# Performance work log

Measured on AMD Instinct MI355X. Metric: run time of the kernel, lower is better.

## Reference

```python
import jax, jax.numpy as jnp
import numpy as np

TOP_K = 2  # hard-coded in MoCo.__init__ (self.top_k = 2)


def setup_inputs() -> dict:
    key = jax.random.key(0)
    k1, k2, k3 = jax.random.split(key, 3)
    B, D, E, O = 16384, 4096, 4, 256  # batch, mlp_dim, num_experts, dim
    v_standard = jax.random.normal(k1, (B, D), dtype=jnp.float32)
    router_w = jax.random.normal(k2, (D, E), dtype=jnp.float32) / np.float32(np.sqrt(D))
    expert_w = jax.random.normal(k3, (E, D, O), dtype=jnp.float32) / np.float32(np.sqrt(D))
    return {"v_standard": v_standard, "router_w": router_w, "expert_w": expert_w}


def reference(v_standard, router_w, expert_w):
    # Router + softmax gating: [B, E]
    routing_logits = v_standard @ router_w
    routing_weights = jax.nn.softmax(routing_logits, axis=-1)

    # Top-k gating, renormalized over the selected experts
    topk_weights, topk_indices = jax.lax.top_k(routing_weights, TOP_K)  # [B, k]
    topk_weights = topk_weights / topk_weights.sum(axis=-1, keepdims=True)

    # Dense all-expert compute (as in the original: every expert runs on every token)
    expert_outputs = jnp.einsum('bd,edo->beo', v_standard, expert_w)  # [B, E, O]

    # Gather the top-k expert outputs and combine with gate weights
    selected = jnp.take_along_axis(expert_outputs, topk_indices[:, :, None], axis=1)  # [B, k, O]
    moe_output = (selected * topk_weights[:, :, None]).sum(axis=1)  # [B, O]
    return moe_output, routing_weights
```

## Files before the change

### kernel.cpp

```cpp
#include <hip/hip_runtime.h>

typedef unsigned short ushort_t;
typedef __attribute__((ext_vector_type(8))) short short8;
typedef __attribute__((ext_vector_type(4))) float floatx4;
typedef __attribute__((ext_vector_type(4))) unsigned int uint4v;

static __device__ __forceinline__ unsigned short f2bf_rn(float f) {
  return (unsigned short)((__float_as_uint(f) + 0x8000u) >> 16);
}
static __device__ __forceinline__ unsigned int packbf(float a, float b) {
  return ((__float_as_uint(a) + 0x8000u) >> 16) |
         ((__float_as_uint(b) + 0x8000u) & 0xFFFF0000u);
}

__global__ __launch_bounds__(256) void k_transpose(const float* __restrict__ We,
                                                   ushort_t* __restrict__ WT) {
  __shared__ float tile[32][33];
  int t = threadIdx.x, tx = t & 31, ty = t >> 5;
  int d0 = blockIdx.x * 32, o0 = blockIdx.y * 32, e = blockIdx.z;
  const float* src = We + (size_t)e * 4096 * 256;
  ushort_t* dst = WT + (size_t)e * 256 * 4096;
#pragma unroll
  for (int r = 0; r < 4; ++r)
    tile[ty + r * 8][tx] = src[(size_t)(d0 + ty + r * 8) * 256 + (o0 + tx)];
  __syncthreads();
#pragma unroll
  for (int r = 0; r < 4; ++r)
    dst[(size_t)(o0 + ty + r * 8) * 4096 + (d0 + tx)] = f2bf_rn(tile[tx][ty + r * 8]);
}

__global__ __launch_bounds__(256) void k_prep_router(const float* __restrict__ Wr,
                                                     float* __restrict__ WrT32) {
  int d = blockIdx.x * 256 + threadIdx.x;
  float4 w = *(const float4*)(Wr + (size_t)d * 4);
  WrT32[d] = w.x;
  WrT32[4096 + d] = w.y;
  WrT32[2 * 4096 + d] = w.z;
  WrT32[3 * 4096 + d] = w.w;
}

__global__ __launch_bounds__(256) void k_routing(const float* __restrict__ V,
                                                 const float* __restrict__ WrT32,
                                                 float* __restrict__ rw_out,
                                                 float* __restrict__ gates) {
  int w = threadIdx.x >> 6, lane = threadIdx.x & 63;
  int b = blockIdx.x * 4 + w;
  const float* vrow = V + (size_t)b * 4096;
  float a0 = 0.f, a1 = 0.f, a2 = 0.f, a3 = 0.f;
#pragma unroll
  for (int j = 0; j < 16; ++j) {
    int d = j * 256 + lane * 4;
    float4 vv = *(const float4*)(vrow + d);
    float4 w0 = *(const float4*)(WrT32 + d);
    float4 w1 = *(const float4*)(WrT32 + 4096 + d);
    float4 w2 = *(const float4*)(WrT32 + 2 * 4096 + d);
    float4 w3 = *(const float4*)(WrT32 + 3 * 4096 + d);
    a0 += vv.x * w0.x + vv.y * w0.y + vv.z * w0.z + vv.w * w0.w;
    a1 += vv.x * w1.x + vv.y * w1.y + vv.z * w1.z + vv.w * w1.w;
    a2 += vv.x * w2.x + vv.y * w2.y + vv.z * w2.z + vv.w * w2.w;
    a3 += vv.x * w3.x + vv.y * w3.y + vv.z * w3.z + vv.w * w3.w;
  }
#pragma unroll
  for (int mask = 1; mask < 64; mask <<= 1) {
    a0 += __shfl_xor(a0, mask, 64);
    a1 += __shfl_xor(a1, mask, 64);
    a2 += __shfl_xor(a2, mask, 64);
    a3 += __shfl_xor(a3, mask, 64);
  }
  float mx = fmaxf(fmaxf(a0, a1), fmaxf(a2, a3));
  float e0 = expf(a0 - mx), e1 = expf(a1 - mx), e2 = expf(a2 - mx), e3 = expf(a3 - mx);
  float s = e0 + e1 + e2 + e3;
  float p[4] = {e0 / s, e1 / s, e2 / s, e3 / s};
  int i1 = 0;
#pragma unroll
  for (int k = 1; k < 4; ++k)
    if (p[k] > p[i1]) i1 = k;
  int i2 = (i1 == 0) ? 1 : 0;
#pragma unroll
  for (int k = 0; k < 4; ++k)
    if (k != i1 && p[k] > p[i2]) i2 = k;
  float gs = p[i1] + p[i2];
  if (lane < 4) {
    rw_out[(size_t)b * 4 + lane] = p[lane];
    gates[(size_t)b * 4 + lane] = (lane == i1 || lane == i2) ? (p[lane] / gs) : 0.f;
  }
}

#define BM 128
#define BN 64
#define BK 64

__global__ __launch_bounds__(256, 2) void k_gemm_moe(const float* __restrict__ V,
                                                     const ushort_t* __restrict__ WT,
                                                     const float* __restrict__ gates,
                                                     float* __restrict__ out) {
  const int Kd = 4096;
  int bn = blockIdx.x;
  int bm = blockIdx.y;
  int m0 = bm * BM, n0 = bn * BN;

  __shared__ __align__(16) ushort_t Asm[BM * BK];
  __shared__ __align__(16) ushort_t Bsm[4 * BN * BK];

  int t = threadIdx.x;
  int w = t >> 6, lane = t & 63;
  int quad = lane >> 4, mi = lane & 15;
  int wm = (w >> 1) * 64, wn = (w & 1) * 32;

  int aG[4], aL[4];
#pragma unroll
  for (int j = 0; j < 4; ++j) {
    int q = j * 256 + t;
    int row = q >> 3, c = q & 7;
    aG[j] = (m0 + row) * Kd + c * 8;
    aL[j] = (row * 8 + (c ^ (row & 7))) * 8;
  }
  int bG[8], bL[8];
#pragma unroll
  for (int j = 0; j < 8; ++j) {
    int q = j * 256 + t;
    int eb = q >> 9, rc = q & 511;
    int r = rc >> 3, c = rc & 7;
    bG[j] = eb * (256 * Kd) + (n0 + r) * Kd + c * 8;
    bL[j] = eb * (BN * BK) + (r * 8 + (c ^ (r & 7))) * 8;
  }

  int aOff[2][4], bOff[2][2];
#pragma unroll
  for (int k32 = 0; k32 < 2; ++k32) {
    int cc = k32 * 4 + quad;
#pragma unroll
    for (int i = 0; i < 4; ++i) {
      int rowa = wm + i * 16 + mi;
      aOff[k32][i] = (rowa * 8 + (cc ^ (rowa & 7))) * 8;
    }
#pragma unroll
    for (int j = 0; j < 2; ++j) {
      int rowb = wn + j * 16 + mi;
      bOff[k32][j] = (rowb * 8 + (cc ^ (rowb & 7))) * 8;
    }
  }

  floatx4 zero = {0.f, 0.f, 0.f, 0.f};
  floatx4 acc[4][4][2];
#pragma unroll
  for (int e = 0; e < 4; ++e)
#pragma unroll
    for (int i = 0; i < 4; ++i)
#pragma unroll
      for (int j = 0; j < 2; ++j) acc[e][i][j] = zero;

  float4 ax[4], ay[4];
  short8 bv[8];
#pragma unroll
  for (int j = 0; j < 4; ++j) {
    const float* ap = V + (size_t)aG[j];
    ax[j] = *(const float4*)ap;
    ay[j] = *(const float4*)(ap + 4);
  }
#pragma unroll
  for (int j = 0; j < 8; ++j) bv[j] = *(const short8*)(WT + (size_t)bG[j]);

  for (int kt = 0; kt < Kd / BK; ++kt) {
#pragma unroll
    for (int j = 0; j < 4; ++j) {
      uint4v uv;
      uv.x = packbf(ax[j].x, ax[j].y);
      uv.y = packbf(ax[j].z, ax[j].w);
      uv.z = packbf(ay[j].x, ay[j].y);
      uv.w = packbf(ay[j].z, ay[j].w);
      *(uint4v*)(Asm + aL[j]) = uv;
    }
#pragma unroll
    for (int j = 0; j < 8; ++j) *(short8*)(Bsm + bL[j]) = bv[j];
    __syncthreads();

    if (kt + 1 < Kd / BK) {
      int k0n = (kt + 1) * BK;
#pragma unroll
      for (int j = 0; j < 4; ++j) {
        const float* ap = V + (size_t)(aG[j] + k0n);
        ax[j] = *(const float4*)ap;
        ay[j] = *(const float4*)(ap + 4);
      }
#pragma unroll
      for (int j = 0; j < 8; ++j) bv[j] = *(const short8*)(WT + (size_t)(bG[j] + k0n));
    }

#pragma unroll
    for (int k32 = 0; k32 < 2; ++k32) {
      short8 af[4];
#pragma unroll
      for (int i = 0; i < 4; ++i) af[i] = *(const short8*)(Asm + aOff[k32][i]);
#pragma unroll
      for (int e = 0; e < 4; ++e) {
        short8 bfr[2];
#pragma unroll
        for (int j = 0; j < 2; ++j)
          bfr[j] = *(const short8*)(Bsm + e * (BN * BK) + bOff[k32][j]);
#pragma unroll
        for (int i = 0; i < 4; ++i)
#pragma unroll
          for (int j = 0; j < 2; ++j)
            acc[e][i][j] =
                __builtin_amdgcn_mfma_f32_16x16x32_bf16(af[i], bfr[j], acc[e][i][j], 0, 0, 0);
      }
    }
    __syncthreads();
  }

#pragma unroll
  for (int i = 0; i < 4; ++i) {
#pragma unroll
    for (int r = 0; r < 4; ++r) {
      int m = m0 + wm + i * 16 + quad * 4 + r;
      float4 gv = *(const float4*)(gates + (size_t)m * 4);
#pragma unroll
      for (int j = 0; j < 2; ++j) {
        float sv = gv.x * acc[0][i][j][r] + gv.y * acc[1][i][j][r] +
                   gv.z * acc[2][i][j][r] + gv.w * acc[3][i][j][r];
        out[(size_t)m * 256 + n0 + wn + j * 16 + mi] = sv;
      }
    }
  }
}

extern "C" void kernel_launch(void* const* d_in, const int* in_sizes, int n_in,
                              void* d_out, int out_size, void* d_ws, size_t ws_size,
                              hipStream_t stream) {
  const float* V = (const float*)d_in[0];
  const float* Wr = (const float*)d_in[1];
  const float* We = (const float*)d_in[2];

  float* out_moe = (float*)d_out;
  float* out_rw = out_moe + (size_t)16384 * 256;

  char* ws = (char*)d_ws;
  float* gates = (float*)ws;
  ushort_t* WT = (ushort_t*)(ws + 262144);
  float* WrT32 = (float*)(ws + 262144 + 8388608);

  k_transpose<<<dim3(128, 8, 4), 256, 0, stream>>>(We, WT);
  k_prep_router<<<dim3(16), 256, 0, stream>>>(Wr, WrT32);
  k_routing<<<dim3(4096), 256, 0, stream>>>(V, WrT32, out_rw, gates);
  k_gemm_moe<<<dim3(4, 128), 256, 0, stream>>>(V, WT, gates, out_moe);
}
```

Measured before the change: 599.5 us.

## Pre-convert activations to bf16 in routing and stream GEMM tiles via direct global-to-LDS loads

The routing kernel now also writes a bf16 copy of V into workspace, so the GEMM reads half the bytes and no longer converts fp32 to bf16 inside its main loop. The new GEMM loads A and B tiles straight into LDS with the global_load_lds builtin, keeping the XOR swizzle. It uses 512-thread blocks, each wave owning a smaller 32x32 tile, and remaps block indices so blocks are grouped across XCDs. This costs an extra 128MB bf16 write, and the loop now has no register prefetch, so load latency is exposed between the two barriers. It falls back to the old path when the workspace is too small.

```diff
diff --git a/kernel.cpp b/kernel.cpp
--- a/kernel.cpp
+++ b/kernel.cpp
@@ -11,6 +11,11 @@
 static __device__ __forceinline__ unsigned int packbf(float a, float b) {
   return ((__float_as_uint(a) + 0x8000u) >> 16) |
          ((__float_as_uint(b) + 0x8000u) & 0xFFFF0000u);
+}
+static __device__ __forceinline__ void gld_lds16(const void* g, void* l) {
+  __builtin_amdgcn_global_load_lds(
+      (const __attribute__((address_space(1))) unsigned int*)g,
+      (__attribute__((address_space(3))) unsigned int*)l, 16, 0, 0);
 }
 
 __global__ __launch_bounds__(256) void k_transpose(const float* __restrict__ We,
@@ -39,15 +44,17 @@
   WrT32[3 * 4096 + d] = w.w;
 }
 
-__global__ __launch_bounds__(256) void k_routing(const float* __restrict__ V,
-                                                 const float* __restrict__ WrT32,
-                                                 float* __restrict__ rw_out,
-                                                 float* __restrict__ gates) {
+__global__ __launch_bounds__(256) void k_routing2(const float* __restrict__ V,
+                                                  const float* __restrict__ WrT32,
+                                                  float* __restrict__ rw_out,
+                                                  float* __restrict__ gates,
+                                                  ushort_t* __restrict__ Vh) {
   int w = threadIdx.x >> 6, lane = threadIdx.x & 63;
   int b = blockIdx.x * 4 + w;
   const float* vrow = V + (size_t)b * 4096;
+  ushort_t* vhrow = Vh + (size_t)b * 4096;
   float a0 = 0.f, a1 = 0.f, a2 = 0.f, a3 = 0.f;
-#pragma unroll
+#pragma unroll 4
   for (int j = 0; j < 16; ++j) {
     int d = j * 256 + lane * 4;
     float4 vv = *(const float4*)(vrow + d);
@@ -59,6 +66,170 @@
     a1 += vv.x * w1.x + vv.y * w1.y + vv.z * w1.z + vv.w * w1.w;
     a2 += vv.x * w2.x + vv.y * w2.y + vv.z * w2.z + vv.w * w2.w;
     a3 += vv.x * w3.x + vv.y * w3.y + vv.z * w3.z + vv.w * w3.w;
+    uint2 pk;
+    pk.x = packbf(vv.x, vv.y);
+    pk.y = packbf(vv.z, vv.w);
+    *(uint2*)(vhrow + d) = pk;
+  }
+#pragma unroll
+  for (int mask = 1; mask < 64; mask <<= 1) {
+    a0 += __shfl_xor(a0, mask, 64);
+    a1 += __shfl_xor(a1, mask, 64);
+    a2 += __shfl_xor(a2, mask, 64);
+    a3 += __shfl_xor(a3, mask, 64);
+  }
+  float mx = fmaxf(fmaxf(a0, a1), fmaxf(a2, a3));
+  float e0 = expf(a0 - mx), e1 = expf(a1 - mx), e2 = expf(a2 - mx), e3 = expf(a3 - mx);
+  float s = e0 + e1 + e2 + e3;
+  float p[4] = {e0 / s, e1 / s, e2 / s, e3 / s};
+  int i1 = 0;
+#pragma unroll
+  for (int k = 1; k < 4; ++k)
+    if (p[k] > p[i1]) i1 = k;
+  int i2 = (i1 == 0) ? 1 : 0;
+#pragma unroll
+  for (int k = 0; k < 4; ++k)
+    if (k != i1 && p[k] > p[i2]) i2 = k;
+  float gs = p[i1] + p[i2];
+  if (lane < 4) {
+    rw_out[(size_t)b * 4 + lane] = p[lane];
+    gates[(size_t)b * 4 + lane] = (lane == i1 || lane == i2) ? (p[lane] / gs) : 0.f;
+  }
+}
+
+#define BM2 128
+#define BN2 64
+#define BK2 64
+
+__global__ __launch_bounds__(512, 4) void k_gemm2(const ushort_t* __restrict__ Vh,
+                                                  const ushort_t* __restrict__ WT,
+                                                  const float* __restrict__ gates,
+                                                  float* __restrict__ out) {
+  const int Kd = 4096;
+  int g = blockIdx.x;
+  int xcd = g & 7, slot = g >> 3;
+  int bm = xcd + ((slot >> 2) << 3);
+  int bn = slot & 3;
+  int m0 = bm * BM2, n0 = bn * BN2;
+
+  __shared__ __align__(16) ushort_t Asm[BM2 * BK2];
+  __shared__ __align__(16) ushort_t Bsm[4 * BN2 * BK2];
+
+  int t = threadIdx.x;
+  int w = t >> 6, lane = t & 63;
+  int quad = lane >> 4, mi = lane & 15;
+  int wm = (w >> 1) * 32, wn = (w & 1) * 32;
+
+  size_t aSrc[2];
+  int aDst[2];
+#pragma unroll
+  for (int s = 0; s < 2; ++s) {
+    int q = (w * 2 + s) * 64 + lane;
+    int row = q >> 3, c = (q & 7) ^ (row & 7);
+    aSrc[s] = (size_t)(m0 + row) * Kd + c * 8;
+    aDst[s] = (w * 2 + s) * 512;
+  }
+  size_t bSrc[4];
+  int bDst[4];
+#pragma unroll
+  for (int s = 0; s < 4; ++s) {
+    int q = (w * 4 + s) * 64 + lane;
+    int e = q >> 9, r = (q >> 3) & 63, c = (q & 7) ^ (r & 7);
+    bSrc[s] = (size_t)e * 256 * Kd + (size_t)(n0 + r) * Kd + c * 8;
+    bDst[s] = (w * 4 + s) * 512;
+  }
+
+  int aOff[2][2], bOff[2][2];
+#pragma unroll
+  for (int k32 = 0; k32 < 2; ++k32) {
+    int cc = k32 * 4 + quad;
+#pragma unroll
+    for (int i = 0; i < 2; ++i) {
+      int ra = wm + i * 16 + mi;
+      aOff[k32][i] = (ra * 8 + (cc ^ (ra & 7))) * 8;
+    }
+#pragma unroll
+    for (int j = 0; j < 2; ++j) {
+      int rb = wn + j * 16 + mi;
+      bOff[k32][j] = (rb * 8 + (cc ^ (rb & 7))) * 8;
+    }
+  }
+
+  floatx4 zero = {0.f, 0.f, 0.f, 0.f};
+  floatx4 acc[4][2][2];
+#pragma unroll
+  for (int e = 0; e < 4; ++e)
+#pragma unroll
+    for (int i = 0; i < 2; ++i)
+#pragma unroll
+      for (int j = 0; j < 2; ++j) acc[e][i][j] = zero;
+
+  for (int kt = 0; kt < Kd / BK2; ++kt) {
+    size_t k0 = (size_t)kt * BK2;
+#pragma unroll
+    for (int s = 0; s < 2; ++s) gld_lds16(Vh + aSrc[s] + k0, Asm + aDst[s]);
+#pragma unroll
+    for (int s = 0; s < 4; ++s) gld_lds16(WT + bSrc[s] + k0, Bsm + bDst[s]);
+    __syncthreads();
+
+#pragma unroll
+    for (int k32 = 0; k32 < 2; ++k32) {
+      short8 af[2];
+#pragma unroll
+      for (int i = 0; i < 2; ++i) af[i] = *(const short8*)(Asm + aOff[k32][i]);
+#pragma unroll
+      for (int e = 0; e < 4; ++e) {
+        short8 bfr[2];
+#pragma unroll
+        for (int j = 0; j < 2; ++j)
+          bfr[j] = *(const short8*)(Bsm + e * (BN2 * BK2) + bOff[k32][j]);
+#pragma unroll
+        for (int i = 0; i < 2; ++i)
+#pragma unroll
+          for (int j = 0; j < 2; ++j)
+            acc[e][i][j] =
+                __builtin_amdgcn_mfma_f32_16x16x32_bf16(af[i], bfr[j], acc[e][i][j], 0, 0, 0);
+      }
+    }
+    __syncthreads();
+  }
+
+#pragma unroll
+  for (int i = 0; i < 2; ++i) {
+#pragma unroll
+    for (int r = 0; r < 4; ++r) {
+      int m = m0 + wm + i * 16 + quad * 4 + r;
+      float4 gv = *(const float4*)(gates + (size_t)m * 4);
+#pragma unroll
+      for (int j = 0; j < 2; ++j) {
+        float sv = gv.x * acc[0][i][j][r] + gv.y * acc[1][i][j][r] +
+                   gv.z * acc[2][i][j][r] + gv.w * acc[3][i][j][r];
+        out[(size_t)m * 256 + n0 + wn + j * 16 + mi] = sv;
+      }
+    }
+  }
+}
+
+__global__ __launch_bounds__(256) void k_routing(const float* __restrict__ V,
+                                                 const float* __restrict__ WrT32,
+                                                 float* __restrict__ rw_out,
+                                                 float* __restrict__ gates) {
+  int w = threadIdx.x >> 6, lane = threadIdx.x & 63;
+  int b = blockIdx.x * 4 + w;
+  const float* vrow = V + (size_t)b * 4096;
+  float a0 = 0.f, a1 = 0.f, a2 = 0.f, a3 = 0.f;
+#pragma unroll
+  for (int j = 0; j < 16; ++j) {
+    int d = j * 256 + lane * 4;
+    float4 vv = *(const float4*)(vrow + d);
+    float4 w0 = *(const float4*)(WrT32 + d);
+    float4 w1 = *(const float4*)(WrT32 + 4096 + d);
+    float4 w2 = *(const float4*)(WrT32 + 2 * 4096 + d);
+    float4 w3 = *(const float4*)(WrT32 + 3 * 4096 + d);
+    a0 += vv.x * w0.x + vv.y * w0.y + vv.z * w0.z + vv.w * w0.w;
+    a1 += vv.x * w1.x + vv.y * w1.y + vv.z * w1.z + vv.w * w1.w;
+    a2 += vv.x * w2.x + vv.y * w2.y + vv.z * w2.z + vv.w * w2.w;
+    a3 += vv.x * w3.x + vv.y * w3.y + vv.z * w3.z + vv.w * w3.w;
   }
 #pragma unroll
   for (int mask = 1; mask < 64; mask <<= 1) {
@@ -239,9 +410,17 @@
   float* gates = (float*)ws;
   ushort_t* WT = (ushort_t*)(ws + 262144);
   float* WrT32 = (float*)(ws + 262144 + 8388608);
+  ushort_t* Vh = (ushort_t*)(ws + 262144 + 8388608 + 65536);
+  size_t need = 262144ull + 8388608ull + 65536ull + 16384ull * 4096ull * 2ull;
 
   k_transpose<<<dim3(128, 8, 4), 256, 0, stream>>>(We, WT);
   k_prep_router<<<dim3(16), 256, 0, stream>>>(Wr, WrT32);
-  k_routing<<<dim3(4096), 256, 0, stream>>>(V, WrT32, out_rw, gates);
-  k_gemm_moe<<<dim3(4, 128), 256, 0, stream>>>(V, WT, gates, out_moe);
-}
+
+  if (ws_size >= need) {
+    k_routing2<<<dim3(4096), 256, 0, stream>>>(V, WrT32, out_rw, gates, Vh);
+    k_gemm2<<<dim3(512), 512, 0, stream>>>(Vh, WT, gates, out_moe);
+  } else {
+    k_routing<<<dim3(4096), 256, 0, stream>>>(V, WrT32, out_rw, gates);
+    k_gemm_moe<<<dim3(4, 128), 256, 0, stream>>>(V, WT, gates, out_moe);
+  }
+}
```

Measured after the change: 527.5 us. -12.0%, faster.
